# Optimization experiments

Measured on AMD Instinct MI355X. Metric: run time of the kernel, lower is better.

Reference implementation:

```python
import jax, jax.numpy as jnp
import numpy as np

N_NODES = 50000
N_EDGES = 400000
D_IN, D_HID, D_OUT = 512, 512, 256


def setup_inputs() -> dict:
    key = jax.random.key(0)
    k = jax.random.split(key, 6)
    x = jax.random.normal(k[0], (N_NODES, D_IN), dtype=jnp.float32)
    edge_index = jax.random.randint(k[1], (2, N_EDGES), 0, N_NODES, dtype=jnp.int64)
    # Glorot-ish init for the two GCNConv linear layers
    W1 = jax.random.normal(k[2], (D_IN, D_HID), dtype=jnp.float32) * (1.0 / np.sqrt(D_IN))
    b1 = jnp.zeros((D_HID,), dtype=jnp.float32)
    W2 = jax.random.normal(k[3], (D_HID, D_OUT), dtype=jnp.float32) * (1.0 / np.sqrt(D_HID))
    b2 = jnp.zeros((D_OUT,), dtype=jnp.float32)
    return {"x": x, "edge_index": edge_index, "W1": W1, "b1": b1, "W2": W2, "b2": b2}


def _gcn_conv(x, W, b, src, dst, norm, n):
    """PyG GCNConv: h = x W; out[i] = sum_{j->i} norm_e * h[j] + b.
    src/dst already include self-loops; norm = d^-1/2[src] * d^-1/2[dst]."""
    h = x @ W  # [n, d_out]
    msgs = h[src] * norm[:, None]  # gather + scale per edge
    agg = jnp.zeros((n, h.shape[1]), dtype=h.dtype).at[dst].add(msgs)  # scatter-add
    return agg + b


def reference(x, edge_index, W1, b1, W2, b2):
    n = x.shape[0]
    loop = jnp.arange(n, dtype=edge_index.dtype)
    src = jnp.concatenate([edge_index[0], loop])  # add self-loops
    dst = jnp.concatenate([edge_index[1], loop])
    # symmetric normalization on the self-loop-augmented graph
    deg = jnp.zeros((n,), dtype=x.dtype).at[dst].add(1.0)
    dinv = jnp.where(deg > 0, jax.lax.rsqrt(deg), 0.0)
    norm = dinv[src] * dinv[dst]
    h = jax.nn.relu(_gcn_conv(x, W1, b1, src, dst, norm, n))
    return _gcn_conv(h, W2, b2, src, dst, norm, n)
```

## Files before the change

kernel.cpp:

```cpp
#include <hip/hip_runtime.h>
#include <stdint.h>

typedef __bf16 bf16_t;
typedef __bf16 bf16x8 __attribute__((ext_vector_type(8)));
typedef float f32x4 __attribute__((ext_vector_type(4)));
typedef uint32_t u32x4 __attribute__((ext_vector_type(4)));

#define N_NODES  50000
#define N_EDGES  400000
#define D_IN     512
#define D_HID    512
#define D_OUTD   256
#define M_PAD    50048
#define NB_SCAN  196

__device__ __forceinline__ uint32_t f2bf_bits(float x){
    uint32_t u = __float_as_uint(x);
    return (u + 0x7fffu + ((u >> 16) & 1u)) >> 16;
}
__device__ __forceinline__ void unpack8(uint4 v, float* f){
    f[0]=__uint_as_float(v.x<<16); f[1]=__uint_as_float(v.x & 0xffff0000u);
    f[2]=__uint_as_float(v.y<<16); f[3]=__uint_as_float(v.y & 0xffff0000u);
    f[4]=__uint_as_float(v.z<<16); f[5]=__uint_as_float(v.z & 0xffff0000u);
    f[6]=__uint_as_float(v.w<<16); f[7]=__uint_as_float(v.w & 0xffff0000u);
}
__device__ __forceinline__ void glds16(const bf16_t* g, bf16_t* l){
    __builtin_amdgcn_global_load_lds(
        (const __attribute__((address_space(1))) uint32_t*)g,
        (__attribute__((address_space(3))) uint32_t*)l, 16, 0, 0);
}

__global__ __launch_bounds__(256)
void conv_x_bf16(const float* __restrict__ x, bf16_t* __restrict__ Xb,
                 int* __restrict__ deg){
    const int t = blockIdx.x * 256 + threadIdx.x;
    if (t < N_NODES) deg[t] = 1;
    const int row = t >> 7;
    uint2 o;
    if (row < N_NODES){
        f32x4 v = __builtin_nontemporal_load(((const f32x4*)x) + t);
        o.x = f2bf_bits(v.x) | (f2bf_bits(v.y) << 16);
        o.y = f2bf_bits(v.z) | (f2bf_bits(v.w) << 16);
    } else { o.x = 0u; o.y = 0u; }
    ((uint2*)Xb)[t] = o;
}

__global__ __launch_bounds__(256)
void conv_w_both(const float* __restrict__ W1, const float* __restrict__ W2,
                 bf16_t* __restrict__ W1t, bf16_t* __restrict__ W2t,
                 const int* __restrict__ ei, int* __restrict__ deg){
    const int idx = blockIdx.x * 256 + threadIdx.x;
    if (idx < N_EDGES) atomicAdd(&deg[ei[N_EDGES + idx]], 1);
    const int n = idx >> 9;
    const int k = idx & 511;
    if (n < 512) W1t[idx] = (bf16_t)W1[k * 512 + n];
    else if (n < 768) W2t[(n - 512) * 512 + k] = (bf16_t)W2[k * 256 + (n - 512)];
}

__global__ __launch_bounds__(256)
void k_scan_dinv(const int* __restrict__ deg, float* __restrict__ dinv,
                 int* __restrict__ part, int* __restrict__ bsum, int n){
    __shared__ int tmp[256];
    int i = blockIdx.x*256 + threadIdx.x;
    int d = (i < n) ? deg[i] : 1;
    if (i < n) dinv[i] = rsqrtf((float)d);
    int v = (i < n) ? (d - 1) : 0;
    tmp[threadIdx.x] = v;
    __syncthreads();
    for (int off = 1; off < 256; off <<= 1){
        int t = (threadIdx.x >= off) ? tmp[threadIdx.x - off] : 0;
        __syncthreads();
        tmp[threadIdx.x] += t;
        __syncthreads();
    }
    if (i < n) part[i] = tmp[threadIdx.x] - v;
    if (threadIdx.x == 255) bsum[blockIdx.x] = tmp[255];
}
__global__ __launch_bounds__(256)
void k_scan_bsum(const int* __restrict__ bsum, int* __restrict__ bsum2, int nb){
    __shared__ int tmp[256];
    int v = (threadIdx.x < nb) ? bsum[threadIdx.x] : 0;
    tmp[threadIdx.x] = v;
    __syncthreads();
    for (int off = 1; off < 256; off <<= 1){
        int t = (threadIdx.x >= off) ? tmp[threadIdx.x - off] : 0;
        __syncthreads();
        tmp[threadIdx.x] += t;
        __syncthreads();
    }
    if (threadIdx.x < nb) bsum2[threadIdx.x] = tmp[threadIdx.x] - v;
}
__global__ __launch_bounds__(256)
void k_finalize_rowptr(const int* __restrict__ part, const int* __restrict__ bsum2,
                       int* __restrict__ rowp, int* __restrict__ cursor, int n){
    int i = blockIdx.x*256 + threadIdx.x;
    if (i < n){ int r = part[i] + bsum2[blockIdx.x]; rowp[i] = r; cursor[i] = r; }
    if (i == 0) rowp[n] = N_EDGES;
}
__global__ __launch_bounds__(256)
void k_place(const int* __restrict__ ei, const float* __restrict__ dinv,
             int* __restrict__ cursor, int* __restrict__ csrc, float* __restrict__ cnorm){
    int e = blockIdx.x*256 + threadIdx.x;
    if (e < N_EDGES){
        int s = ei[e];
        int d = ei[N_EDGES + e];
        int p = atomicAdd(&cursor[d], 1);
        csrc[p]  = s;
        cnorm[p] = dinv[s] * dinv[d];
    }
}

__global__ __launch_bounds__(256, 2)
void gemm_bf16_mfma(const bf16_t* __restrict__ A, const bf16_t* __restrict__ Bt,
                    bf16_t* __restrict__ C, int N, int K)
{
    __shared__ bf16_t As[2][128*32];
    __shared__ bf16_t Bs[2][128*32];

    const int tid  = threadIdx.x;
    const int wave = tid >> 6;
    const int lane = tid & 63;
    const int wr = wave >> 1;
    const int wc = wave & 1;
    const int mBase = blockIdx.x * 128;
    const int nBase = blockIdx.y * 128;

    const int srow = lane >> 2;
    const int scol = (lane & 3) << 3;
    const bf16_t* Ag0 = A  + (size_t)(mBase + wave*16 + srow) * K + scol;
    const bf16_t* Ag1 = Ag0 + (size_t)64 * K;
    const bf16_t* Bg0 = Bt + (size_t)(nBase + wave*16 + srow) * K + scol;
    const bf16_t* Bg1 = Bg0 + (size_t)64 * K;

    const int m16 = lane & 15;
    const int q   = lane >> 4;
    const int aOff = (wr*64 + m16)*32 + q*8;
    const int bOff = (wc*64 + m16)*32 + q*8;

    f32x4 acc[4][4] = {};

    {
        bf16_t* As0 = &As[0][wave*512];
        bf16_t* Bs0 = &Bs[0][wave*512];
        glds16(Ag0, As0);
        glds16(Ag1, As0 + 64*32);
        glds16(Bg0, Bs0);
        glds16(Bg1, Bs0 + 64*32);
    }

    int cur = 0;
    for (int k0 = 0; k0 < K; k0 += 32){
        __syncthreads();
        if (k0 + 32 < K){
            bf16_t* As1 = &As[cur^1][wave*512];
            bf16_t* Bs1 = &Bs[cur^1][wave*512];
            glds16(Ag0 + k0 + 32, As1);
            glds16(Ag1 + k0 + 32, As1 + 64*32);
            glds16(Bg0 + k0 + 32, Bs1);
            glds16(Bg1 + k0 + 32, Bs1 + 64*32);
        }
        const bf16_t* aP = &As[cur][aOff];
        const bf16_t* bP = &Bs[cur][bOff];
        bf16x8 a[4], b[4];
        #pragma unroll
        for (int t = 0; t < 4; ++t){
            a[t] = *(const bf16x8*)(aP + t*16*32);
            b[t] = *(const bf16x8*)(bP + t*16*32);
        }
        #pragma unroll
        for (int i = 0; i < 4; ++i){
            #pragma unroll
            for (int j = 0; j < 4; ++j){
                acc[i][j] = __builtin_amdgcn_mfma_f32_16x16x32_bf16(a[i], b[j], acc[i][j], 0, 0, 0);
            }
        }
        cur ^= 1;
    }

    #pragma unroll
    for (int i = 0; i < 4; ++i){
        const int row0 = mBase + wr*64 + i*16 + q*4;
        #pragma unroll
        for (int j = 0; j < 4; ++j){
            const int col = nBase + wc*64 + j*16 + m16;
            bf16_t* Cp = C + (size_t)row0 * N + col;
            #pragma unroll
            for (int r = 0; r < 4; ++r)
                Cp[(size_t)r * N] = (bf16_t)acc[i][j][r];
        }
    }
}

__global__ __launch_bounds__(256)
void agg_bias_relu_512(const bf16_t* __restrict__ T, const int* __restrict__ rowp,
                       const int* __restrict__ csrc, const float* __restrict__ cnorm,
                       const float* __restrict__ dinv, const float* __restrict__ bias,
                       bf16_t* __restrict__ H)
{
    const int gw   = (blockIdx.x * 256 + threadIdx.x) >> 6;
    const int lane = threadIdx.x & 63;
    if (gw >= N_NODES) return;
    const float di = dinv[gw];
    float acc[8];
    {
        uint4 v = ((const uint4*)(T + (size_t)gw * 512))[lane];
        float f[8]; unpack8(v, f);
        const float w = di * di;
        #pragma unroll
        for (int j = 0; j < 8; ++j) acc[j] = w * f[j];
    }
    int e = rowp[gw];
    const int e1 = rowp[gw + 1];
    for (; e + 4 <= e1; e += 4){
        const int   s0 = csrc[e],   s1 = csrc[e+1], s2 = csrc[e+2], s3 = csrc[e+3];
        const float w0 = cnorm[e],  w1 = cnorm[e+1], w2 = cnorm[e+2], w3 = cnorm[e+3];
        uint4 v0 = ((const uint4*)(T + (size_t)s0 * 512))[lane];
        uint4 v1 = ((const uint4*)(T + (size_t)s1 * 512))[lane];
        uint4 v2 = ((const uint4*)(T + (size_t)s2 * 512))[lane];
        uint4 v3 = ((const uint4*)(T + (size_t)s3 * 512))[lane];
        float f[8];
        unpack8(v0, f);
        #pragma unroll
        for (int j = 0; j < 8; ++j) acc[j] += w0 * f[j];
        unpack8(v1, f);
        #pragma unroll
        for (int j = 0; j < 8; ++j) acc[j] += w1 * f[j];
        unpack8(v2, f);
        #pragma unroll
        for (int j = 0; j < 8; ++j) acc[j] += w2 * f[j];
        unpack8(v3, f);
        #pragma unroll
        for (int j = 0; j < 8; ++j) acc[j] += w3 * f[j];
    }
    for (; e < e1; ++e){
        const int   s = csrc[e];
        const float w = cnorm[e];
        uint4 v = ((const uint4*)(T + (size_t)s * 512))[lane];
        float f[8]; unpack8(v, f);
        #pragma unroll
        for (int j = 0; j < 8; ++j) acc[j] += w * f[j];
    }
    const float4 b0 = ((const float4*)bias)[lane*2];
    const float4 b1 = ((const float4*)bias)[lane*2 + 1];
    float r[8] = {acc[0]+b0.x, acc[1]+b0.y, acc[2]+b0.z, acc[3]+b0.w,
                  acc[4]+b1.x, acc[5]+b1.y, acc[6]+b1.z, acc[7]+b1.w};
    u32x4 o;
    o.x = f2bf_bits(fmaxf(r[0],0.f)) | (f2bf_bits(fmaxf(r[1],0.f)) << 16);
    o.y = f2bf_bits(fmaxf(r[2],0.f)) | (f2bf_bits(fmaxf(r[3],0.f)) << 16);
    o.z = f2bf_bits(fmaxf(r[4],0.f)) | (f2bf_bits(fmaxf(r[5],0.f)) << 16);
    o.w = f2bf_bits(fmaxf(r[6],0.f)) | (f2bf_bits(fmaxf(r[7],0.f)) << 16);
    __builtin_nontemporal_store(o, ((u32x4*)(H + (size_t)gw * 512)) + lane);
}

__global__ __launch_bounds__(256)
void agg_bias_out_256(const bf16_t* __restrict__ T, const int* __restrict__ rowp,
                      const int* __restrict__ csrc, const float* __restrict__ cnorm,
                      const float* __restrict__ dinv, const float* __restrict__ bias,
                      float* __restrict__ out)
{
    const int wid  = (blockIdx.x * 256 + threadIdx.x) >> 6;
    const int half = (threadIdx.x >> 5) & 1;
    const int l32  = threadIdx.x & 31;
    const int node = wid * 2 + half;
    if (node >= N_NODES) return;
    const float di = dinv[node];
    float acc[8];
    {
        uint4 v = ((const uint4*)(T + (size_t)node * 256))[l32];
        float f[8]; unpack8(v, f);
        const float w = di * di;
        #pragma unroll
        for (int j = 0; j < 8; ++j) acc[j] = w * f[j];
    }
    int e = rowp[node];
    const int e1 = rowp[node + 1];
    for (; e + 4 <= e1; e += 4){
        const int   s0 = csrc[e],   s1 = csrc[e+1], s2 = csrc[e+2], s3 = csrc[e+3];
        const float w0 = cnorm[e],  w1 = cnorm[e+1], w2 = cnorm[e+2], w3 = cnorm[e+3];
        uint4 v0 = ((const uint4*)(T + (size_t)s0 * 256))[l32];
        uint4 v1 = ((const uint4*)(T + (size_t)s1 * 256))[l32];
        uint4 v2 = ((const uint4*)(T + (size_t)s2 * 256))[l32];
        uint4 v3 = ((const uint4*)(T + (size_t)s3 * 256))[l32];
        float f[8];
        unpack8(v0, f);
        #pragma unroll
        for (int j = 0; j < 8; ++j) acc[j] += w0 * f[j];
        unpack8(v1, f);
        #pragma unroll
        for (int j = 0; j < 8; ++j) acc[j] += w1 * f[j];
        unpack8(v2, f);
        #pragma unroll
        for (int j = 0; j < 8; ++j) acc[j] += w2 * f[j];
        unpack8(v3, f);
        #pragma unroll
        for (int j = 0; j < 8; ++j) acc[j] += w3 * f[j];
    }
    for (; e < e1; ++e){
        const int   s = csrc[e];
        const float w = cnorm[e];
        uint4 v = ((const uint4*)(T + (size_t)s * 256))[l32];
        float f[8]; unpack8(v, f);
        #pragma unroll
        for (int j = 0; j < 8; ++j) acc[j] += w * f[j];
    }
    const float4 b0 = ((const float4*)bias)[l32*2];
    const float4 b1 = ((const float4*)bias)[l32*2 + 1];
    f32x4 o0 = {acc[0]+b0.x, acc[1]+b0.y, acc[2]+b0.z, acc[3]+b0.w};
    f32x4 o1 = {acc[4]+b1.x, acc[5]+b1.y, acc[6]+b1.z, acc[7]+b1.w};
    __builtin_nontemporal_store(o0, ((f32x4*)(out + (size_t)node * 256)) + l32*2);
    __builtin_nontemporal_store(o1, ((f32x4*)(out + (size_t)node * 256)) + l32*2 + 1);
}

extern "C" void kernel_launch(void* const* d_in, const int* in_sizes, int n_in,
                              void* d_out, int out_size, void* d_ws, size_t ws_size,
                              hipStream_t stream)
{
    const float* x  = (const float*)d_in[0];
    const int*   ei = (const int*)d_in[1];
    const float* W1 = (const float*)d_in[2];
    const float* b1 = (const float*)d_in[3];
    const float* W2 = (const float*)d_in[4];
    const float* b2 = (const float*)d_in[5];
    float* out = (float*)d_out;

    char* w = (char*)d_ws;
    auto alloc = [&](size_t bytes) -> char* {
        char* p = w; w += (bytes + 255) & ~(size_t)255; return p;
    };
    bf16_t* Xb    = (bf16_t*)alloc((size_t)M_PAD * 512 * 2);
    bf16_t* T     = (bf16_t*)alloc((size_t)M_PAD * 512 * 2);
    bf16_t* W1t   = (bf16_t*)alloc(512 * 512 * 2);
    bf16_t* W2t   = (bf16_t*)alloc(256 * 512 * 2);
    int*    deg   = (int*)  alloc(N_NODES * 4);
    float*  dinv  = (float*)alloc(N_NODES * 4);
    int*    rowp  = (int*)  alloc((N_NODES + 1) * 4);
    int*    cursor= (int*)  alloc(N_NODES * 4);
    int*    part  = (int*)  alloc(N_NODES * 4);
    int*    bsum  = (int*)  alloc(NB_SCAN * 4);
    int*    bsum2 = (int*)  alloc(NB_SCAN * 4);
    int*    csrc  = (int*)  alloc(N_EDGES * 4);
    float*  cnorm = (float*)alloc(N_EDGES * 4);

    conv_x_bf16<<<(M_PAD*128)/256, 256, 0, stream>>>(x, Xb, deg);
    conv_w_both<<<1568, 256, 0, stream>>>(W1, W2, W1t, W2t, ei, deg);

    k_scan_dinv<<<NB_SCAN, 256, 0, stream>>>(deg, dinv, part, bsum, N_NODES);
    k_scan_bsum <<<1, 256, 0, stream>>>(bsum, bsum2, NB_SCAN);
    k_finalize_rowptr<<<NB_SCAN, 256, 0, stream>>>(part, bsum2, rowp, cursor, N_NODES);
    k_place   <<<(N_EDGES+255)/256, 256, 0, stream>>>(ei, dinv, cursor, csrc, cnorm);

    gemm_bf16_mfma<<<dim3(M_PAD/128, 512/128), 256, 0, stream>>>(Xb, W1t, T, 512, 512);
    agg_bias_relu_512<<<(N_NODES+3)/4, 256, 0, stream>>>(T, rowp, csrc, cnorm, dinv, b1, Xb);

    gemm_bf16_mfma<<<dim3(M_PAD/128, 256/128), 256, 0, stream>>>(Xb, W2t, T, 256, 512);
    agg_bias_out_256<<<(25000+3)/4, 256, 0, stream>>>(T, rowp, csrc, cnorm, dinv, b2, out);
}
```

Baseline: 396.5 us.

## Deepen GEMM K-tile to 64 with XOR-swizzled LDS and explicit vmcnt pipelining

The bf16 MFMA GEMM now stages a 64-wide K slice per iteration instead of 32, which halves the number of barrier/iteration overheads. LDS writes use an XOR swizzle on the column chunk so that ds_read of the fragment rows avoids bank conflicts. Prefetch of the next tile is overlapped with compute using explicit s_waitcnt vmcnt and sched_barriers. LDS usage doubles to 64KB per block, which may reduce occupancy from the 2 blocks requested by launch bounds.

Result: no change. 396.5 us (+0.0%).

```diff
diff --git a/kernel.cpp b/kernel.cpp
--- a/kernel.cpp
+++ b/kernel.cpp
@@ -114,8 +114,8 @@
 void gemm_bf16_mfma(const bf16_t* __restrict__ A, const bf16_t* __restrict__ Bt,
                     bf16_t* __restrict__ C, int N, int K)
 {
-    __shared__ bf16_t As[2][128*32];
-    __shared__ bf16_t Bs[2][128*32];
+    __shared__ bf16_t As[2][128*64];
+    __shared__ bf16_t Bs[2][128*64];
 
     const int tid  = threadIdx.x;
     const int wave = tid >> 6;
@@ -125,61 +125,72 @@
     const int mBase = blockIdx.x * 128;
     const int nBase = blockIdx.y * 128;
 
-    const int srow = lane >> 2;
-    const int scol = (lane & 3) << 3;
-    const bf16_t* Ag0 = A  + (size_t)(mBase + wave*16 + srow) * K + scol;
-    const bf16_t* Ag1 = Ag0 + (size_t)64 * K;
-    const bf16_t* Bg0 = Bt + (size_t)(nBase + wave*16 + srow) * K + scol;
-    const bf16_t* Bg1 = Bg0 + (size_t)64 * K;
+    const int sr = lane >> 3;
+    const int sc = (lane & 7) ^ sr;
+    const bf16_t* Asrc[4]; const bf16_t* Bsrc[4];
+    #pragma unroll
+    for (int r = 0; r < 4; ++r){
+        const int row = r*32 + wave*8 + sr;
+        Asrc[r] = A  + (size_t)(mBase + row) * K + sc*8;
+        Bsrc[r] = Bt + (size_t)(nBase + row) * K + sc*8;
+    }
+
+    auto stage = [&](int k0, int p){
+        bf16_t* Ad = &As[p][0];
+        bf16_t* Bd = &Bs[p][0];
+        #pragma unroll
+        for (int r = 0; r < 4; ++r) glds16(Asrc[r] + k0, Ad + (r*256 + tid)*8);
+        #pragma unroll
+        for (int r = 0; r < 4; ++r) glds16(Bsrc[r] + k0, Bd + (r*256 + tid)*8);
+    };
 
     const int m16 = lane & 15;
-    const int q   = lane >> 4;
-    const int aOff = (wr*64 + m16)*32 + q*8;
-    const int bOff = (wc*64 + m16)*32 + q*8;
+    const int q8  = (lane >> 4) << 3;
+    const int swz = (m16 & 7) << 3;
+    const int aBase = (wr*64 + m16)*64;
+    const int bBase = (wc*64 + m16)*64;
 
     f32x4 acc[4][4] = {};
 
-    {
-        bf16_t* As0 = &As[0][wave*512];
-        bf16_t* Bs0 = &Bs[0][wave*512];
-        glds16(Ag0, As0);
-        glds16(Ag1, As0 + 64*32);
-        glds16(Bg0, Bs0);
-        glds16(Bg1, Bs0 + 64*32);
-    }
-
-    int cur = 0;
-    for (int k0 = 0; k0 < K; k0 += 32){
-        __syncthreads();
-        if (k0 + 32 < K){
-            bf16_t* As1 = &As[cur^1][wave*512];
-            bf16_t* Bs1 = &Bs[cur^1][wave*512];
-            glds16(Ag0 + k0 + 32, As1);
-            glds16(Ag1 + k0 + 32, As1 + 64*32);
-            glds16(Bg0 + k0 + 32, Bs1);
-            glds16(Bg1 + k0 + 32, Bs1 + 64*32);
+    stage(0, 0);
+    const int KT = K >> 6;
+    for (int kt = 0; kt < KT; ++kt){
+        const int p = kt & 1;
+        __builtin_amdgcn_s_barrier();
+        __builtin_amdgcn_sched_barrier(0);
+        if (kt + 1 < KT){
+            stage((kt + 1) << 6, p ^ 1);
+            asm volatile("s_waitcnt vmcnt(8)" ::: "memory");
+        } else {
+            asm volatile("s_waitcnt vmcnt(0)" ::: "memory");
         }
-        const bf16_t* aP = &As[cur][aOff];
-        const bf16_t* bP = &Bs[cur][bOff];
-        bf16x8 a[4], b[4];
-        #pragma unroll
-        for (int t = 0; t < 4; ++t){
-            a[t] = *(const bf16x8*)(aP + t*16*32);
-            b[t] = *(const bf16x8*)(bP + t*16*32);
-        }
-        #pragma unroll
-        for (int i = 0; i < 4; ++i){
+        __builtin_amdgcn_sched_barrier(0);
+        __builtin_amdgcn_s_barrier();
+        const bf16_t* Ab = &As[p][0];
+        const bf16_t* Bb = &Bs[p][0];
+        #pragma unroll
+        for (int kk = 0; kk < 2; ++kk){
+            const int ko = (kk*32 + q8) ^ swz;
+            bf16x8 a[4], b[4];
             #pragma unroll
-            for (int j = 0; j < 4; ++j){
-                acc[i][j] = __builtin_amdgcn_mfma_f32_16x16x32_bf16(a[i], b[j], acc[i][j], 0, 0, 0);
+            for (int t = 0; t < 4; ++t){
+                a[t] = *(const bf16x8*)(Ab + aBase + t*1024 + ko);
+                b[t] = *(const bf16x8*)(Bb + bBase + t*1024 + ko);
+            }
+            #pragma unroll
+            for (int i = 0; i < 4; ++i){
+                #pragma unroll
+                for (int j = 0; j < 4; ++j){
+                    acc[i][j] = __builtin_amdgcn_mfma_f32_16x16x32_bf16(a[i], b[j], acc[i][j], 0, 0, 0);
+                }
             }
         }
-        cur ^= 1;
-    }
-
+    }
+
+    const int qr = lane >> 4;
     #pragma unroll
     for (int i = 0; i < 4; ++i){
-        const int row0 = mBase + wr*64 + i*16 + q*4;
+        const int row0 = mBase + wr*64 + i*16 + qr*4;
         #pragma unroll
         for (int j = 0; j < 4; ++j){
             const int col = nBase + wc*64 + j*16 + m16;
```
